# Kernel optimization log

Hardware: AMD Instinct MI355X
Metric: run time of the kernel (lower is better)

## Reference

```python
import jax, jax.numpy as jnp
import numpy as np
from jax import lax

INPUT_DIM = 512
KERNEL_DIM = 3
HEADS = 8
B, L = 16, 1024


def setup_inputs() -> dict:
    key = jax.random.key(0)
    ks = jax.random.split(key, 4)
    fan = INPUT_DIM * KERNEL_DIM
    std = float(np.sqrt(2.0 / (INPUT_DIM + fan)))  # xavier_normal for conv weight
    x = jax.random.normal(ks[0], (B, INPUT_DIM, L), dtype=jnp.float32)
    w0 = jax.random.normal(ks[1], (INPUT_DIM, INPUT_DIM, KERNEL_DIM), dtype=jnp.float32) * std
    w1 = jax.random.normal(ks[2], (INPUT_DIM, INPUT_DIM, KERNEL_DIM), dtype=jnp.float32) * std
    w2 = jax.random.normal(ks[3], (INPUT_DIM, INPUT_DIM, KERNEL_DIM), dtype=jnp.float32) * std
    b0 = jnp.zeros((INPUT_DIM,), jnp.float32)
    b1 = jnp.zeros((INPUT_DIM,), jnp.float32)
    b2 = jnp.zeros((INPUT_DIM,), jnp.float32)
    return {"x": x, "w0": w0, "b0": b0, "w1": w1, "b1": b1, "w2": w2, "b2": b2}


def _conv1d(x, w, b):
    # x: [B, C, L], w: [O, I, K] -> [B, O, L-K+1] (VALID, stride 1)
    y = lax.conv_general_dilated(x, w, window_strides=(1,), padding='VALID',
                                 dimension_numbers=('NCH', 'OIH', 'NCH'))
    return y + b[None, :, None]


def _multihead_attention(q, k, v, input_dim, heads):
    # q,k,v: [B, D, Lp]; chunk along channel dim == reshape to [B, H, Dh, Lp]
    b, d, lp = q.shape
    dh = d // heads
    qh = q.reshape(b, heads, dh, lp)
    kh = k.reshape(b, heads, dh, lp)
    vh = v.reshape(b, heads, dh, lp)
    scale = 1.0 / np.sqrt(input_dim)  # NOTE: original scales by sqrt(full input_dim)
    scores = jnp.einsum('bhdq,bhdk->bhqk', qh, kh) * scale  # [B,H,Lp,Lp]
    attn = jax.nn.softmax(scores, axis=-1)
    out = jnp.einsum('bhqk,bhdk->bhdq', attn, vh)  # [B,H,Dh,Lp]
    return out.reshape(b, d, lp)


def reference(x, w0, b0, w1, b1, w2, b2):
    q = _conv1d(x, w0, b0)
    k = _conv1d(x, w1, b1)
    v = _conv1d(x, w2, b2)
    return _multihead_attention(q, k, v, INPUT_DIM, HEADS)
```

## Files before the change

kernel.cpp:

```cpp
#include <hip/hip_runtime.h>

#define B_SZ 16
#define CIN  512
#define LIN  1024
#define LP   1022
#define HEADS 8
#define DH    64

typedef __attribute__((ext_vector_type(8))) short bf16x8;
typedef __attribute__((ext_vector_type(4))) float f32x4;
typedef __attribute__((ext_vector_type(16))) float f32x16;

__device__ inline unsigned short f2bf(float f) {
    union { float f; unsigned int u; } c; c.f = f;
    unsigned int r = c.u + 0x7FFF + ((c.u >> 16) & 1);
    return (unsigned short)(r >> 16);
}

__device__ __forceinline__ void gl_lds16(const unsigned short* g, unsigned short* l) {
    __builtin_amdgcn_global_load_lds((const __attribute__((address_space(1))) void*)g,
                                     (__attribute__((address_space(3))) void*)l, 16, 0, 0);
}

#define SWZ(G) ((G) ^ (((G) >> 3) & 7))

__global__ __launch_bounds__(256) void xb_cvt_kernel(const float* __restrict__ x,
                                                     unsigned short* __restrict__ xb) {
    __shared__ float sm[64][68];
    const int t  = threadIdx.x;
    const int l0 = blockIdx.x * 64;
    const int i0 = blockIdx.y * 64;
    const int b  = blockIdx.z;
    const float* S = x + ((size_t)b * CIN + i0) * LIN;

    #pragma unroll
    for (int rr = 0; rr < 4; rr++) {
        int idx = rr * 1024 + t * 4;
        int ii = idx >> 6, lj = idx & 63;
        *(float4*)&sm[ii][lj] = *(const float4*)(S + (size_t)ii * LIN + l0 + lj);
    }
    __syncthreads();

    #pragma unroll
    for (int rr = 0; rr < 4; rr++) {
        int idx = rr * 1024 + t * 4;
        int l = idx >> 6, dj = idx & 63;
        ushort4 h;
        h.x = f2bf(sm[dj + 0][l]);
        h.y = f2bf(sm[dj + 1][l]);
        h.z = f2bf(sm[dj + 2][l]);
        h.w = f2bf(sm[dj + 3][l]);
        *(ushort4*)(xb + ((size_t)b * 1024 + l0 + l) * 512 + i0 + dj) = h;
    }
}

__global__ __launch_bounds__(256) void wb_cvt_kernel(const float* __restrict__ w0,
                                                     const float* __restrict__ w1,
                                                     const float* __restrict__ w2,
                                                     unsigned short* __restrict__ wb) {
    const int kk = blockIdx.y;
    int flat = blockIdx.x * 256 + threadIdx.x;
    int i  = flat & 511;
    int oG = flat >> 9;
    int c  = oG >> 9, o = oG & 511;
    const float* w = (c == 0) ? w0 : (c == 1) ? w1 : w2;
    wb[(size_t)kk * 786432 + flat] = f2bf(w[o * 1536 + i * 3 + kk]);
}

__global__ __launch_bounds__(256) void conv_mfma_kernel(
        const unsigned short* __restrict__ xb,
        const unsigned short* __restrict__ wb,
        const float* __restrict__ b0, const float* __restrict__ b1,
        const float* __restrict__ b2,
        unsigned short* __restrict__ Qt, unsigned short* __restrict__ Kt,
        unsigned short* __restrict__ Vt, float qscale) {
    __shared__ unsigned short smem[16896];
    unsigned short* xs = smem;
    unsigned short* ws = smem + 4224;

    const int t    = threadIdx.x;
    const int wave = t >> 6;
    const int lane = t & 63;
    const int col  = lane & 15;
    const int quad = lane >> 4;
    const int wh   = wave >> 1;
    const int wn   = wave & 1;
    const int l0   = blockIdx.x * 128;
    const int o0   = blockIdx.y * 128;
    const int b    = blockIdx.z;

    f32x4 acc[4][4];
    #pragma unroll
    for (int i = 0; i < 4; i++)
        #pragma unroll
        for (int j = 0; j < 4; j++) acc[i][j] = (f32x4){0.f, 0.f, 0.f, 0.f};

    const unsigned short* xrow = xb + (size_t)b * 1024 * 512;

    for (int ic = 0; ic < 512; ic += 32) {
        __syncthreads();

        #pragma unroll
        for (int j = 0; j < 6; j++) {
            int instr = wave * 6 + j;
            int Gg = SWZ(instr * 64 + lane);
            int p = Gg >> 2, q = Gg & 3;
            int kk = p >> 7, orow = p & 127;
            gl_lds16(wb + ((size_t)(kk * 1536 + o0 + orow)) * 512 + ic + q * 8,
                     ws + instr * 512);
        }
        #pragma unroll
        for (int j = 0; j < 2; j++) {
            int instr = wave * 2 + j;
            int Gg = SWZ(instr * 64 + lane);
            int p = Gg >> 2, q = Gg & 3;
            gl_lds16(xrow + (size_t)(l0 + p) * 512 + ic + q * 8,
                     xs + instr * 512);
        }
        if (t < 8) {
            int row = 128 + (t >> 2), sg = t & 3;
            int gl = l0 + row;
            bf16x8 v = (bf16x8){0, 0, 0, 0, 0, 0, 0, 0};
            if (gl < 1024) v = *(const bf16x8*)(xrow + (size_t)gl * 512 + ic + sg * 8);
            *(bf16x8*)&xs[SWZ(512 + t) * 8] = v;
        }
        __syncthreads();

        #pragma unroll
        for (int kk = 0; kk < 3; kk++) {
            bf16x8 af[4], bfr[4];
            #pragma unroll
            for (int ms = 0; ms < 4; ms++) {
                int G = ((kk * 128 + wh * 64 + ms * 16 + col) << 2) | quad;
                af[ms] = *(const bf16x8*)&ws[SWZ(G) * 8];
            }
            #pragma unroll
            for (int ns = 0; ns < 4; ns++) {
                int G = ((wn * 64 + ns * 16 + col + kk) << 2) | quad;
                bfr[ns] = *(const bf16x8*)&xs[SWZ(G) * 8];
            }
            #pragma unroll
            for (int ms = 0; ms < 4; ms++)
                #pragma unroll
                for (int ns = 0; ns < 4; ns++)
                    acc[ms][ns] = __builtin_amdgcn_mfma_f32_16x16x32_bf16(af[ms], bfr[ns], acc[ms][ns], 0, 0, 0);
        }
    }

    const int c = blockIdx.y >> 2;

    if (c < 2) {
        unsigned short* dst = (c == 0) ? Qt : Kt;
        const float* bias   = (c == 0) ? b0 : b1;
        const float sc      = (c == 0) ? qscale : 1.0f;
        const int h = (((o0 & 511) + wh * 64) >> 6) & 7;
        unsigned short* base = dst + (size_t)(b * 8 + h) * 65536;
        #pragma unroll
        for (int ms = 0; ms < 4; ms++) {
            int ob = (o0 & 511) + wh * 64 + ms * 16 + quad * 4;
            float bv[4];
            #pragma unroll
            for (int r = 0; r < 4; r++) bv[r] = bias[ob + r];
            int d0 = ms * 16 + quad * 4;
            #pragma unroll
            for (int ns = 0; ns < 4; ns++) {
                int l = l0 + wn * 64 + ns * 16 + col;
                ushort4 hv;
                hv.x = f2bf((acc[ms][ns][0] + bv[0]) * sc);
                hv.y = f2bf((acc[ms][ns][1] + bv[1]) * sc);
                hv.z = f2bf((acc[ms][ns][2] + bv[2]) * sc);
                hv.w = f2bf((acc[ms][ns][3] + bv[3]) * sc);
                *(ushort4*)(base + (size_t)l * 64 + d0) = hv;
            }
        }
    } else {
        __syncthreads();
        unsigned short* vt = smem;
        #pragma unroll
        for (int ms = 0; ms < 4; ms++) {
            int ob = (o0 & 511) + wh * 64 + ms * 16 + quad * 4;
            #pragma unroll
            for (int ns = 0; ns < 4; ns++) {
                int lc = wn * 64 + ns * 16 + col;
                #pragma unroll
                for (int r = 0; r < 4; r++)
                    vt[(wh * 64 + ms * 16 + quad * 4 + r) * 132 + lc] =
                        f2bf(acc[ms][ns][r] + b2[ob + r]);
            }
        }
        __syncthreads();
        #pragma unroll
        for (int it = 0; it < 8; it++) {
            int flat = it * 2048 + t * 8;
            int row = flat >> 7, colx = flat & 127;
            bf16x8 v = *(const bf16x8*)&vt[row * 132 + colx];
            int og = (o0 & 511) + row;
            int h = og >> 6, d = og & 63;
            *(bf16x8*)(Vt + ((size_t)(b * 8 + h) * 64 + d) * 1024 + l0 + colx) = v;
        }
    }
}

__global__ __launch_bounds__(256, 3) void attn_kernel(
        const unsigned short* __restrict__ Qt,
        const unsigned short* __restrict__ Kt,
        const unsigned short* __restrict__ Vt,
        float* __restrict__ out) {
    __shared__ unsigned short asmem[16384];

    const int t    = threadIdx.x;
    const int wave = t >> 6;
    const int lane = t & 63;
    const int col5 = lane & 31;
    const int hi   = lane >> 5;

    const int lin = blockIdx.y * 8 + blockIdx.x;
    const int xcd = lin & 7;
    const int idx = lin >> 3;
    const int qb  = idx >> 4;
    const int bh  = xcd * 16 + (idx & 15);

    const size_t base64 = (size_t)bh * 65536;
    const int q0 = qb * 128 + wave * 32;

    bf16x8 bq[4];
    {
        const unsigned short* qrow = Qt + base64 + (size_t)(q0 + col5) * 64 + hi * 8;
        #pragma unroll
        for (int s = 0; s < 4; s++) bq[s] = *(const bf16x8*)(qrow + s * 16);
    }

    f32x16 o0, o1;
    #pragma unroll
    for (int i = 0; i < 16; i++) { o0[i] = 0.f; o1[i] = 0.f; }
    float osum = 0.f;

    const unsigned short* kg0 = Kt + base64;
    const unsigned short* vg  = Vt + base64;

    #pragma unroll
    for (int j = 0; j < 2; j++) {
        int i = wave + j * 4;
        int G = SWZ(i * 64 + lane);
        gl_lds16(kg0 + (size_t)G * 8, asmem + i * 512);
        int p = G >> 3, q = G & 7;
        gl_lds16(vg + (size_t)p * 1024 + q * 8, asmem + 4096 + i * 512);
    }
    asm volatile("s_waitcnt vmcnt(0)" ::: "memory");
    __builtin_amdgcn_s_barrier();
    asm volatile("" ::: "memory");

    int cur = 0;
    for (int kt = 0; kt < 16; kt++) {
        if (kt < 15) {
            const unsigned short* kg = kg0 + (size_t)(kt + 1) * 4096;
            unsigned short* Kb = asmem + (cur ^ 1) * 8192;
            #pragma unroll
            for (int j = 0; j < 2; j++) {
                int i = wave + j * 4;
                int G = SWZ(i * 64 + lane);
                gl_lds16(kg + (size_t)G * 8, Kb + i * 512);
                int p = G >> 3, q = G & 7;
                gl_lds16(vg + (size_t)p * 1024 + (kt + 1) * 64 + q * 8,
                         Kb + 4096 + i * 512);
            }
        }

        const unsigned short* Ksb = asmem + cur * 8192;
        const unsigned short* Vsb = Ksb + 4096;

        #pragma unroll
        for (int kb = 0; kb < 2; kb++) {
            bf16x8 ak[4];
            #pragma unroll
            for (int s = 0; s < 4; s++)
                ak[s] = *(const bf16x8*)&Ksb[SWZ((kb * 32 + col5) * 8 + s * 2 + hi) * 8];
            bf16x8 av[2][2];
            #pragma unroll
            for (int db = 0; db < 2; db++)
                #pragma unroll
                for (int s = 0; s < 2; s++)
                    av[db][s] = *(const bf16x8*)&Vsb[SWZ((db * 32 + col5) * 8 + kb * 4 + s * 2 + hi) * 8];

            f32x16 p;
            #pragma unroll
            for (int i = 0; i < 16; i++) p[i] = 0.f;
            __builtin_amdgcn_s_setprio(1);
            #pragma unroll
            for (int s = 0; s < 4; s++)
                p = __builtin_amdgcn_mfma_f32_32x32x16_bf16(ak[s], bq[s], p, 0, 0, 0);
            __builtin_amdgcn_s_setprio(0);

            float e[16];
            #pragma unroll
            for (int r = 0; r < 16; r++) e[r] = exp2f(p[r]);
            if (kt == 15 && kb == 1 && hi == 1) { e[14] = 0.f; e[15] = 0.f; }
            #pragma unroll
            for (int r = 0; r < 16; r++) osum += e[r];

            bf16x8 bp[2];
            #pragma unroll
            for (int s = 0; s < 2; s++) {
                unsigned int a, b_, c, d;
                asm("v_cvt_pk_bf16_f32 %0, %1, %2" : "=v"(a)  : "v"(e[s*8+0]), "v"(e[s*8+1]));
                asm("v_cvt_pk_bf16_f32 %0, %1, %2" : "=v"(b_) : "v"(e[s*8+2]), "v"(e[s*8+3]));
                asm("v_cvt_pk_bf16_f32 %0, %1, %2" : "=v"(c)  : "v"(e[s*8+4]), "v"(e[s*8+5]));
                asm("v_cvt_pk_bf16_f32 %0, %1, %2" : "=v"(d)  : "v"(e[s*8+6]), "v"(e[s*8+7]));
                unsigned int as = (unsigned int)__shfl_xor((int)a,  32);
                unsigned int bs = (unsigned int)__shfl_xor((int)b_, 32);
                unsigned int cs = (unsigned int)__shfl_xor((int)c,  32);
                unsigned int ds = (unsigned int)__shfl_xor((int)d,  32);
                union { unsigned int u[4]; bf16x8 v; } pk;
                pk.u[0] = hi ? cs : a;
                pk.u[1] = hi ? ds : b_;
                pk.u[2] = hi ? c  : as;
                pk.u[3] = hi ? d  : bs;
                bp[s] = pk.v;
            }

            __builtin_amdgcn_s_setprio(1);
            #pragma unroll
            for (int s = 0; s < 2; s++) {
                o0 = __builtin_amdgcn_mfma_f32_32x32x16_bf16(av[0][s], bp[s], o0, 0, 0, 0);
                o1 = __builtin_amdgcn_mfma_f32_32x32x16_bf16(av[1][s], bp[s], o1, 0, 0, 0);
            }
            __builtin_amdgcn_s_setprio(0);
        }

        asm volatile("s_waitcnt vmcnt(0)" ::: "memory");
        __builtin_amdgcn_s_barrier();
        asm volatile("" ::: "memory");
        cur ^= 1;
    }

    float osum_t = osum + __shfl_xor(osum, 32);
    float inv = 1.0f / osum_t;
    int q = q0 + col5;
    if (q < LP) {
        #pragma unroll
        for (int r = 0; r < 16; r++) {
            int d0 = (r & 3) + 8 * (r >> 2) + 4 * hi;
            out[((size_t)(bh * 64 + d0)) * LP + q]      = o0[r] * inv;
            out[((size_t)(bh * 64 + d0 + 32)) * LP + q] = o1[r] * inv;
        }
    }
}

extern "C" void kernel_launch(void* const* d_in, const int* in_sizes, int n_in,
                              void* d_out, int out_size, void* d_ws, size_t ws_size,
                              hipStream_t stream) {
    const float* x  = (const float*)d_in[0];
    const float* w0 = (const float*)d_in[1];
    const float* b0 = (const float*)d_in[2];
    const float* w1 = (const float*)d_in[3];
    const float* b1 = (const float*)d_in[4];
    const float* w2 = (const float*)d_in[5];
    const float* b2 = (const float*)d_in[6];
    float* out = (float*)d_out;

    unsigned short* xbp = (unsigned short*)d_ws;
    unsigned short* wbp = xbp + 8388608;
    unsigned short* Qt  = wbp + 2359296;
    unsigned short* Kt  = Qt + 8388608;
    unsigned short* Vt  = Kt + 8388608;

    const float scale = 0.06375870864f;

    xb_cvt_kernel<<<dim3(16, 8, 16), 256, 0, stream>>>(x, xbp);
    wb_cvt_kernel<<<dim3(3072, 3), 256, 0, stream>>>(w0, w1, w2, wbp);
    conv_mfma_kernel<<<dim3(8, 12, 16), 256, 0, stream>>>(xbp, wbp, b0, b1, b2,
                                                          Qt, Kt, Vt, scale);
    attn_kernel<<<dim3(8, 128), 256, 0, stream>>>(Qt, Kt, Vt, out);
}
```

Before: 233.4 us.

## Load K/V fragments directly from global memory and use permlane32 swap

The attention kernel drops the double-buffered LDS staging of K and V tiles, along with its per-tile barriers. Each wave now loads its MFMA operand fragments straight from global memory and relies on L2/cache hits, since four waves share the same K/V. The P-fragment exchange between wave halves switches from four ds-bpermute shuffles plus selects to two v_permlane32_swap instructions. The cost is global load latency that is no longer hidden by explicit prefetch, plus duplicated cache traffic across waves.

```diff
diff --git a/kernel.cpp b/kernel.cpp
--- a/kernel.cpp
+++ b/kernel.cpp
@@ -206,8 +206,6 @@
         const unsigned short* __restrict__ Kt,
         const unsigned short* __restrict__ Vt,
         float* __restrict__ out) {
-    __shared__ unsigned short asmem[16384];
-
     const int t    = threadIdx.x;
     const int wave = t >> 6;
     const int lane = t & 63;
@@ -235,52 +233,23 @@
     for (int i = 0; i < 16; i++) { o0[i] = 0.f; o1[i] = 0.f; }
     float osum = 0.f;
 
-    const unsigned short* kg0 = Kt + base64;
-    const unsigned short* vg  = Vt + base64;
-
-    #pragma unroll
-    for (int j = 0; j < 2; j++) {
-        int i = wave + j * 4;
-        int G = SWZ(i * 64 + lane);
-        gl_lds16(kg0 + (size_t)G * 8, asmem + i * 512);
-        int p = G >> 3, q = G & 7;
-        gl_lds16(vg + (size_t)p * 1024 + q * 8, asmem + 4096 + i * 512);
-    }
-    asm volatile("s_waitcnt vmcnt(0)" ::: "memory");
-    __builtin_amdgcn_s_barrier();
-    asm volatile("" ::: "memory");
-
-    int cur = 0;
+    const unsigned short* kp0 = Kt + base64 + (size_t)col5 * 64 + hi * 8;
+    const unsigned short* vp0 = Vt + base64 + (size_t)col5 * 1024 + hi * 8;
+
     for (int kt = 0; kt < 16; kt++) {
-        if (kt < 15) {
-            const unsigned short* kg = kg0 + (size_t)(kt + 1) * 4096;
-            unsigned short* Kb = asmem + (cur ^ 1) * 8192;
-            #pragma unroll
-            for (int j = 0; j < 2; j++) {
-                int i = wave + j * 4;
-                int G = SWZ(i * 64 + lane);
-                gl_lds16(kg + (size_t)G * 8, Kb + i * 512);
-                int p = G >> 3, q = G & 7;
-                gl_lds16(vg + (size_t)p * 1024 + (kt + 1) * 64 + q * 8,
-                         Kb + 4096 + i * 512);
-            }
-        }
-
-        const unsigned short* Ksb = asmem + cur * 8192;
-        const unsigned short* Vsb = Ksb + 4096;
-
         #pragma unroll
         for (int kb = 0; kb < 2; kb++) {
+            const int k0 = kt * 64 + kb * 32;
+            const unsigned short* kp = kp0 + (size_t)k0 * 64;
             bf16x8 ak[4];
             #pragma unroll
-            for (int s = 0; s < 4; s++)
-                ak[s] = *(const bf16x8*)&Ksb[SWZ((kb * 32 + col5) * 8 + s * 2 + hi) * 8];
+            for (int s = 0; s < 4; s++) ak[s] = *(const bf16x8*)(kp + s * 16);
             bf16x8 av[2][2];
             #pragma unroll
             for (int db = 0; db < 2; db++)
                 #pragma unroll
                 for (int s = 0; s < 2; s++)
-                    av[db][s] = *(const bf16x8*)&Vsb[SWZ((db * 32 + col5) * 8 + kb * 4 + s * 2 + hi) * 8];
+                    av[db][s] = *(const bf16x8*)(vp0 + (size_t)db * 32768 + k0 + s * 16);
 
             f32x16 p;
             #pragma unroll
@@ -306,15 +275,13 @@
                 asm("v_cvt_pk_bf16_f32 %0, %1, %2" : "=v"(b_) : "v"(e[s*8+2]), "v"(e[s*8+3]));
                 asm("v_cvt_pk_bf16_f32 %0, %1, %2" : "=v"(c)  : "v"(e[s*8+4]), "v"(e[s*8+5]));
                 asm("v_cvt_pk_bf16_f32 %0, %1, %2" : "=v"(d)  : "v"(e[s*8+6]), "v"(e[s*8+7]));
-                unsigned int as = (unsigned int)__shfl_xor((int)a,  32);
-                unsigned int bs = (unsigned int)__shfl_xor((int)b_, 32);
-                unsigned int cs = (unsigned int)__shfl_xor((int)c,  32);
-                unsigned int ds = (unsigned int)__shfl_xor((int)d,  32);
+                asm("v_permlane32_swap_b32 %0, %1" : "+v"(a), "+v"(c));
+                asm("v_permlane32_swap_b32 %0, %1" : "+v"(b_), "+v"(d));
                 union { unsigned int u[4]; bf16x8 v; } pk;
-                pk.u[0] = hi ? cs : a;
-                pk.u[1] = hi ? ds : b_;
-                pk.u[2] = hi ? c  : as;
-                pk.u[3] = hi ? d  : bs;
+                pk.u[0] = a;
+                pk.u[1] = b_;
+                pk.u[2] = c;
+                pk.u[3] = d;
                 bp[s] = pk.v;
             }
 
@@ -326,11 +293,6 @@
             }
             __builtin_amdgcn_s_setprio(0);
         }
-
-        asm volatile("s_waitcnt vmcnt(0)" ::: "memory");
-        __builtin_amdgcn_s_barrier();
-        asm volatile("" ::: "memory");
-        cur ^= 1;
     }
 
     float osum_t = osum + __shfl_xor(osum, 32);
```

Result: slower. 294.5 us (+26.2%).
